# Optimization experiments

Measured on AMD Instinct MI355X. Metric: run time of the kernel, lower is better.

## Reference

```python
import jax, jax.numpy as jnp
import numpy as np

LN_EPS = 1e-5

def _layernorm(x, g, b):
    mu = jnp.mean(x, axis=-1, keepdims=True)
    var = jnp.mean(jnp.square(x - mu), axis=-1, keepdims=True)
    return (x - mu) * jax.lax.rsqrt(var + LN_EPS) * g + b


def setup_inputs() -> dict:
    key = jax.random.key(0)
    ks = jax.random.split(key, 8)
    B, N, F = 2, 100000, 128
    E, G = 400000, 10
    EMB, C = 32, 128
    features = jax.random.normal(ks[0], (B, N, F), dtype=jnp.float32)
    edge_index = jax.random.randint(ks[1], (2, E), 0, N, dtype=jnp.int32)
    lengths = jnp.full((G,), N // G, dtype=jnp.int32)
    emb_table = jax.random.normal(ks[2], (128, EMB), dtype=jnp.float32)
    W_in = jax.random.normal(ks[3], (F - 1 + EMB, C), dtype=jnp.float32) * (1.0 / np.sqrt(F - 1 + EMB))
    b_in = jnp.zeros((C,), jnp.float32)
    g_in = jnp.ones((C,), jnp.float32)
    beta_in = jnp.zeros((C,), jnp.float32)
    msg_W = jax.random.normal(ks[4], (3, C, C), dtype=jnp.float32) * (1.0 / np.sqrt(C))
    msg_b = jnp.zeros((3, C), jnp.float32)
    msg_g = jnp.ones((3, C), jnp.float32)
    msg_beta = jnp.zeros((3, C), jnp.float32)
    W_proj = jax.random.normal(ks[5], (C, 1), dtype=jnp.float32) * (1.0 / np.sqrt(C))
    b_proj = jnp.zeros((1,), jnp.float32)
    return {"features": features, "edge_index": edge_index, "lengths": lengths,
            "emb_table": emb_table, "W_in": W_in, "b_in": b_in, "g_in": g_in, "beta_in": beta_in,
            "msg_W": msg_W, "msg_b": msg_b, "msg_g": msg_g, "msg_beta": msg_beta,
            "W_proj": W_proj, "b_proj": b_proj}


def reference(features, edge_index, lengths, emb_table, W_in, b_in, g_in, beta_in,
              msg_W, msg_b, msg_g, msg_beta, W_proj, b_proj):
    B, N, F = features.shape
    rows, cols = edge_index[0], edge_index[1]

    # row-normalized sparse adjacency values (no grad path in original: torch.no_grad)
    ones = jnp.ones(rows.shape[0], dtype=features.dtype)
    deg = jax.ops.segment_sum(ones, rows, num_segments=N)
    vals = 1.0 / jnp.clip(deg, 1.0)[rows]  # [E]
    vals = jax.lax.stop_gradient(vals)

    # embedding input layer
    op = jnp.clip(features[..., 0].astype(jnp.int32), 0, emb_table.shape[0] - 1)  # [B,N]
    x = jnp.concatenate([emb_table[op], features[..., 1:]], axis=-1)  # [B,N,F-1+emb]
    x = _layernorm(jax.nn.silu(x @ W_in + b_in), g_in, beta_in)  # [B,N,C]

    # sparse message passing: agg[i] = sum_j A[i,j] x[j]
    for l in range(msg_W.shape[0]):
        msg = x[:, cols, :] * vals[None, :, None]  # [B,E,C]
        agg = jnp.zeros_like(x).at[:, rows, :].add(msg)  # scatter-sum to rows
        x = _layernorm(jax.nn.silu(agg @ msg_W[l] + msg_b[l]), msg_g[l], msg_beta[l])

    # ragged graph pooling over node axis
    G = lengths.shape[0]
    index = jnp.asarray(np.repeat(np.arange(G), np.asarray(lengths)))  # [N]
    pooled = jax.ops.segment_sum(x.transpose(1, 0, 2), index, num_segments=G)  # [G,B,C]
    runtimes = pooled @ W_proj + b_proj  # [G,B,1]
    return runtimes[..., 0]  # [G,B]
```

## Files before the change

### kernel.cpp

```cpp
#include <hip/hip_runtime.h>
#include <cstddef>

#define LN_EPS 1e-5f
typedef unsigned short u16;
typedef unsigned int u32;
typedef __attribute__((ext_vector_type(8))) short bf16x8;
typedef __attribute__((ext_vector_type(4))) float f32x4;

constexpr int SCAN_T = 256, SCAN_V = 8, SCAN_ELEMS = SCAN_T * SCAN_V;
constexpr int KP = 136;

__device__ inline u16 f2bf(float f) {
    u32 u = __float_as_uint(f);
    u += 0x7FFFu + ((u >> 16) & 1u);
    return (u16)(u >> 16);
}
__device__ inline float bf2f(u16 h) { return __uint_as_float((u32)h << 16); }

__device__ inline void acc_u4(float* a, uint4 u) {
    a[0] += bf2f((u16)(u.x & 0xFFFF)); a[1] += bf2f((u16)(u.x >> 16));
    a[2] += bf2f((u16)(u.y & 0xFFFF)); a[3] += bf2f((u16)(u.y >> 16));
    a[4] += bf2f((u16)(u.z & 0xFFFF)); a[5] += bf2f((u16)(u.z >> 16));
    a[6] += bf2f((u16)(u.w & 0xFFFF)); a[7] += bf2f((u16)(u.w >> 16));
}

__global__ __launch_bounds__(256) void k_deg(const int* __restrict__ rows,
                                             int* __restrict__ deg, int E) {
    int e = blockIdx.x * 256 + threadIdx.x;
    if (e < E) atomicAdd(&deg[rows[e]], 1);
}

__global__ __launch_bounds__(256) void k_invdeg(const int* __restrict__ deg,
                                                float* __restrict__ invdeg, int N) {
    int i = blockIdx.x * 256 + threadIdx.x;
    if (i < N) invdeg[i] = 1.0f / (float)max(deg[i], 1);
}

__global__ __launch_bounds__(SCAN_T) void k_scan1(const int* __restrict__ deg,
                                                  int* __restrict__ row_ptr,
                                                  int* __restrict__ bsum, int N) {
    __shared__ int ts[SCAN_T];
    int t = threadIdx.x;
    int base = blockIdx.x * SCAN_ELEMS;
    int v[SCAN_V];
    int s = 0;
    #pragma unroll
    for (int j = 0; j < SCAN_V; ++j) {
        int i = base + t * SCAN_V + j;
        v[j] = (i < N) ? deg[i] : 0;
        s += v[j];
    }
    ts[t] = s;
    __syncthreads();
    for (int off = 1; off < SCAN_T; off <<= 1) {
        int val = (t >= off) ? ts[t - off] : 0;
        __syncthreads();
        ts[t] += val;
        __syncthreads();
    }
    int excl = (t > 0) ? ts[t - 1] : 0;
    #pragma unroll
    for (int j = 0; j < SCAN_V; ++j) {
        int i = base + t * SCAN_V + j;
        if (i < N) row_ptr[i] = excl;
        excl += v[j];
    }
    if (t == SCAN_T - 1) bsum[blockIdx.x] = ts[SCAN_T - 1];
}

__global__ void k_scan2(int* __restrict__ bsum, int nb, int* __restrict__ row_ptr, int N) {
    int run = 0;
    for (int i = 0; i < nb; ++i) {
        int v = bsum[i];
        bsum[i] = run;
        run += v;
    }
    row_ptr[N] = run;
}

__global__ __launch_bounds__(SCAN_T) void k_scan3(int* __restrict__ row_ptr,
                                                  const int* __restrict__ bsum, int N) {
    int add = bsum[blockIdx.x];
    int base = blockIdx.x * SCAN_ELEMS;
    #pragma unroll
    for (int j = 0; j < SCAN_V; ++j) {
        int i = base + threadIdx.x * SCAN_V + j;
        if (i < N) row_ptr[i] += add;
    }
}

__global__ __launch_bounds__(256) void k_copy_cursor(const int* __restrict__ row_ptr,
                                                     int* __restrict__ cursor, int N) {
    int i = blockIdx.x * 256 + threadIdx.x;
    if (i < N) cursor[i] = row_ptr[i];
}

__global__ __launch_bounds__(256) void k_bucket(const int* __restrict__ rows,
                                                const int* __restrict__ cols,
                                                int* __restrict__ cursor,
                                                int* __restrict__ col_sorted, int E) {
    int e = blockIdx.x * 256 + threadIdx.x;
    if (e < E) {
        int r = rows[e];
        int pos = atomicAdd(&cursor[r], 1);
        col_sorted[pos] = cols[e];
    }
}

__global__ __launch_bounds__(256) void k_wprep(const float* __restrict__ W_in,
                                               const float* __restrict__ msg_W,
                                               u16* __restrict__ Wt_in,
                                               u16* __restrict__ Wt_msg) {
    int idx = blockIdx.x * 256 + threadIdx.x;
    const int t1 = 128 * KP;
    if (idx < t1) {
        int c = idx / KP, k = idx % KP;
        float v = (k >= 1 && k < 128) ? W_in[(31 + k) * 128 + c] : 0.f;
        Wt_in[idx] = f2bf(v);
    } else {
        idx -= t1;
        if (idx < 3 * 128 * KP) {
            int l = idx / (128 * KP);
            int r = idx % (128 * KP);
            int c = r / KP, k = r % KP;
            Wt_msg[idx] = (k < 128) ? f2bf(msg_W[l * 16384 + k * 128 + c]) : (u16)0;
        }
    }
}

__global__ __launch_bounds__(128) void k_eproj(const float* __restrict__ W_in,
                                               const float* __restrict__ emb,
                                               float* __restrict__ E_proj) {
    __shared__ float es[32];
    int op = blockIdx.x, c = threadIdx.x;
    if (c < 32) es[c] = emb[op * 32 + c];
    __syncthreads();
    float s = 0.f;
    #pragma unroll
    for (int j = 0; j < 32; ++j) s = fmaf(es[j], W_in[j * 128 + c], s);
    E_proj[op * 128 + c] = s;
}

__global__ __launch_bounds__(256) void k_input_mfma(
    const float* __restrict__ features, const float* __restrict__ E_proj,
    const u16* __restrict__ Wt,
    const float* __restrict__ bias, const float* __restrict__ gain,
    const float* __restrict__ beta, u16* __restrict__ x, int M, int ntiles)
{
    __shared__ u16 A[64 * KP];
    __shared__ u16 Wl[128 * KP];
    __shared__ int ops[64];
    const int tid = threadIdx.x;
    const int lane = tid & 63, w = tid >> 6;
    const int r = tid >> 2, q = tid & 3;

    {
        const uint4* src = (const uint4*)Wt;
        uint4* dst = (uint4*)Wl;
        const int n16 = 128 * KP / 8;
        for (int i = tid; i < n16; i += 256) dst[i] = src[i];
    }
    float bsr[8], gsr[8], btr[8];
    #pragma unroll
    for (int t = 0; t < 8; ++t) {
        int col = t * 16 + (lane & 15);
        bsr[t] = bias[col]; gsr[t] = gain[col]; btr[t] = beta[col];
    }

    for (int tile = blockIdx.x; tile < ntiles; tile += gridDim.x) {
        const int node0 = tile * 64;
        __syncthreads();
        {
            int rg = min(node0 + r, M - 1);
            const float* fr = features + (size_t)rg * 128 + q * 32;
            u32 pk[16];
            float4 v0 = ((const float4*)fr)[0];
            if (q == 0) {
                int op = (int)v0.x;
                op = op < 0 ? 0 : (op > 127 ? 127 : op);
                ops[r] = op;
            }
            pk[0] = (u32)f2bf(v0.x) | ((u32)f2bf(v0.y) << 16);
            pk[1] = (u32)f2bf(v0.z) | ((u32)f2bf(v0.w) << 16);
            #pragma unroll
            for (int j = 1; j < 8; ++j) {
                float4 v = ((const float4*)fr)[j];
                pk[2 * j]     = (u32)f2bf(v.x) | ((u32)f2bf(v.y) << 16);
                pk[2 * j + 1] = (u32)f2bf(v.z) | ((u32)f2bf(v.w) << 16);
            }
            uint4* dst = (uint4*)&A[r * KP + q * 32];
            #pragma unroll
            for (int j = 0; j < 4; ++j)
                dst[j] = make_uint4(pk[4 * j], pk[4 * j + 1], pk[4 * j + 2], pk[4 * j + 3]);
        }
        __syncthreads();

        const int arow = w * 16 + (lane & 15);
        const int kq = (lane >> 4) * 8;
        bf16x8 a[4];
        #pragma unroll
        for (int kt = 0; kt < 4; ++kt)
            a[kt] = *(const bf16x8*)&A[arow * KP + kt * 32 + kq];
        f32x4 acc[8];
        #pragma unroll
        for (int t = 0; t < 8; ++t) {
            int bcol = t * 16 + (lane & 15);
            f32x4 c4 = {0.f, 0.f, 0.f, 0.f};
            #pragma unroll
            for (int kt = 0; kt < 4; ++kt) {
                bf16x8 b = *(const bf16x8*)&Wl[bcol * KP + kt * 32 + kq];
                c4 = __builtin_amdgcn_mfma_f32_16x16x32_bf16(a[kt], b, c4, 0, 0, 0);
            }
            acc[t] = c4;
        }
        int opr[4];
        #pragma unroll
        for (int i = 0; i < 4; ++i) opr[i] = ops[w * 16 + (lane >> 4) * 4 + i];
        float s[4] = {0, 0, 0, 0}, sq[4] = {0, 0, 0, 0};
        #pragma unroll
        for (int t = 0; t < 8; ++t) {
            int col = t * 16 + (lane & 15);
            #pragma unroll
            for (int i = 0; i < 4; ++i) {
                float aY = acc[t][i] + bsr[t] + E_proj[opr[i] * 128 + col];
                float y = aY / (1.0f + __expf(-aY));
                acc[t][i] = y;
                s[i] += y;
                sq[i] = fmaf(y, y, sq[i]);
            }
        }
        #pragma unroll
        for (int m = 1; m <= 8; m <<= 1) {
            #pragma unroll
            for (int i = 0; i < 4; ++i) {
                s[i] += __shfl_xor(s[i], m);
                sq[i] += __shfl_xor(sq[i], m);
            }
        }
        #pragma unroll
        for (int i = 0; i < 4; ++i) {
            float mu = s[i] * (1.0f / 128.0f);
            float var = sq[i] * (1.0f / 128.0f) - mu * mu;
            float inv = rsqrtf(var + LN_EPS);
            int rg = node0 + w * 16 + (lane >> 4) * 4 + i;
            if (rg < M) {
                u16* xr = x + (size_t)rg * 128;
                #pragma unroll
                for (int t = 0; t < 8; ++t) {
                    int col = t * 16 + (lane & 15);
                    xr[col] = f2bf((acc[t][i] - mu) * inv * gsr[t] + btr[t]);
                }
            }
        }
    }
}

__global__ __launch_bounds__(256) void k_mp_mfma(
    const int* __restrict__ row_ptr, const int* __restrict__ col_sorted,
    const float* __restrict__ invdeg, const u16* __restrict__ xin,
    const u16* __restrict__ Wt, const float* __restrict__ bias,
    const float* __restrict__ gain, const float* __restrict__ beta,
    u16* __restrict__ xout, int N, int M, int ntiles)
{
    __shared__ u16 A[64 * KP];
    __shared__ u16 Wl[128 * KP];
    const int tid = threadIdx.x;
    const int lane = tid & 63, w = tid >> 6;
    const int r = tid >> 2, q = tid & 3;

    {
        const uint4* src = (const uint4*)Wt;
        uint4* dst = (uint4*)Wl;
        const int n16 = 128 * KP / 8;
        for (int i = tid; i < n16; i += 256) dst[i] = src[i];
    }
    float bsr[8], gsr[8], btr[8];
    #pragma unroll
    for (int t = 0; t < 8; ++t) {
        int col = t * 16 + (lane & 15);
        bsr[t] = bias[col]; gsr[t] = gain[col]; btr[t] = beta[col];
    }

    for (int tile = blockIdx.x; tile < ntiles; tile += gridDim.x) {
        const int node0 = tile * 64;
        __syncthreads();
        {
            int rg = min(node0 + r, M - 1);
            int b = rg / N;
            int nrow = rg - b * N;
            int e0 = row_ptr[nrow], e1 = row_ptr[nrow + 1];
            float sc = invdeg[nrow];
            const u32* xb = (const u32*)xin + (size_t)b * N * 64 + q * 16;
            float fa[32];
            #pragma unroll
            for (int j = 0; j < 32; ++j) fa[j] = 0.f;
            int e = e0;
            for (; e + 2 <= e1; e += 2) {
                int c0 = col_sorted[e], c1 = col_sorted[e + 1];
                const uint4* p0 = (const uint4*)(xb + (size_t)c0 * 64);
                const uint4* p1 = (const uint4*)(xb + (size_t)c1 * 64);
                uint4 u0 = p0[0], u1 = p0[1], u2 = p0[2], u3 = p0[3];
                uint4 w0 = p1[0], w1 = p1[1], w2 = p1[2], w3 = p1[3];
                acc_u4(fa + 0, u0);  acc_u4(fa + 8, u1);
                acc_u4(fa + 16, u2); acc_u4(fa + 24, u3);
                acc_u4(fa + 0, w0);  acc_u4(fa + 8, w1);
                acc_u4(fa + 16, w2); acc_u4(fa + 24, w3);
            }
            if (e < e1) {
                const uint4* p0 = (const uint4*)(xb + (size_t)col_sorted[e] * 64);
                uint4 u0 = p0[0], u1 = p0[1], u2 = p0[2], u3 = p0[3];
                acc_u4(fa + 0, u0);  acc_u4(fa + 8, u1);
                acc_u4(fa + 16, u2); acc_u4(fa + 24, u3);
            }
            u32 pk[16];
            #pragma unroll
            for (int j = 0; j < 16; ++j)
                pk[j] = (u32)f2bf(fa[2 * j] * sc) | ((u32)f2bf(fa[2 * j + 1] * sc) << 16);
            uint4* dst = (uint4*)&A[r * KP + q * 32];
            #pragma unroll
            for (int j = 0; j < 4; ++j)
                dst[j] = make_uint4(pk[4 * j], pk[4 * j + 1], pk[4 * j + 2], pk[4 * j + 3]);
        }
        __syncthreads();

        const int arow = w * 16 + (lane & 15);
        const int kq = (lane >> 4) * 8;
        bf16x8 a[4];
        #pragma unroll
        for (int kt = 0; kt < 4; ++kt)
            a[kt] = *(const bf16x8*)&A[arow * KP + kt * 32 + kq];
        f32x4 acc[8];
        #pragma unroll
        for (int t = 0; t < 8; ++t) {
            int bcol = t * 16 + (lane & 15);
            f32x4 c4 = {0.f, 0.f, 0.f, 0.f};
            #pragma unroll
            for (int kt = 0; kt < 4; ++kt) {
                bf16x8 b = *(const bf16x8*)&Wl[bcol * KP + kt * 32 + kq];
                c4 = __builtin_amdgcn_mfma_f32_16x16x32_bf16(a[kt], b, c4, 0, 0, 0);
            }
            acc[t] = c4;
        }
        float s[4] = {0, 0, 0, 0}, sq[4] = {0, 0, 0, 0};
        #pragma unroll
        for (int t = 0; t < 8; ++t) {
            #pragma unroll
            for (int i = 0; i < 4; ++i) {
                float aY = acc[t][i] + bsr[t];
                float y = aY / (1.0f + __expf(-aY));
                acc[t][i] = y;
                s[i] += y;
                sq[i] = fmaf(y, y, sq[i]);
            }
        }
        #pragma unroll
        for (int m = 1; m <= 8; m <<= 1) {
            #pragma unroll
            for (int i = 0; i < 4; ++i) {
                s[i] += __shfl_xor(s[i], m);
                sq[i] += __shfl_xor(sq[i], m);
            }
        }
        #pragma unroll
        for (int i = 0; i < 4; ++i) {
            float mu = s[i] * (1.0f / 128.0f);
            float var = sq[i] * (1.0f / 128.0f) - mu * mu;
            float inv = rsqrtf(var + LN_EPS);
            int rg = node0 + w * 16 + (lane >> 4) * 4 + i;
            if (rg < M) {
                u16* xr = xout + (size_t)rg * 128;
                #pragma unroll
                for (int t = 0; t < 8; ++t) {
                    int col = t * 16 + (lane & 15);
                    xr[col] = f2bf((acc[t][i] - mu) * inv * gsr[t] + btr[t]);
                }
            }
        }
    }
}

__global__ __launch_bounds__(64) void k_pool(
    const u16* __restrict__ x, const int* __restrict__ lengths,
    float* __restrict__ pooled, int N, int B, int G, int SPLIT)
{
    int blk = blockIdx.x;
    int split = blk % SPLIT;
    int gb = blk / SPLIT;
    int b = gb % B, g = gb / B;
    int lane = threadIdx.x;
    int start = 0;
    for (int i = 0; i < g; ++i) start += lengths[i];
    int len = lengths[g];
    int chunk = (len + SPLIT - 1) / SPLIT;
    int n0 = start + split * chunk;
    int n1 = min(start + len, n0 + chunk);
    const u32* xb = (const u32*)x + (size_t)b * N * 64;
    float sx = 0.f, sy = 0.f;
    int n = n0;
    for (; n + 8 <= n1; n += 8) {
        u32 v0 = xb[(size_t)(n + 0) * 64 + lane];
        u32 v1 = xb[(size_t)(n + 1) * 64 + lane];
        u32 v2 = xb[(size_t)(n + 2) * 64 + lane];
        u32 v3 = xb[(size_t)(n + 3) * 64 + lane];
        u32 v4 = xb[(size_t)(n + 4) * 64 + lane];
        u32 v5 = xb[(size_t)(n + 5) * 64 + lane];
        u32 v6 = xb[(size_t)(n + 6) * 64 + lane];
        u32 v7 = xb[(size_t)(n + 7) * 64 + lane];
        sx += bf2f((u16)(v0 & 0xFFFF)) + bf2f((u16)(v1 & 0xFFFF)) +
              bf2f((u16)(v2 & 0xFFFF)) + bf2f((u16)(v3 & 0xFFFF)) +
              bf2f((u16)(v4 & 0xFFFF)) + bf2f((u16)(v5 & 0xFFFF)) +
              bf2f((u16)(v6 & 0xFFFF)) + bf2f((u16)(v7 & 0xFFFF));
        sy += bf2f((u16)(v0 >> 16)) + bf2f((u16)(v1 >> 16)) +
              bf2f((u16)(v2 >> 16)) + bf2f((u16)(v3 >> 16)) +
              bf2f((u16)(v4 >> 16)) + bf2f((u16)(v5 >> 16)) +
              bf2f((u16)(v6 >> 16)) + bf2f((u16)(v7 >> 16));
    }
    for (; n < n1; ++n) {
        u32 v = xb[(size_t)n * 64 + lane];
        sx += bf2f((u16)(v & 0xFFFF));
        sy += bf2f((u16)(v >> 16));
    }
    if (n1 > n0) {
        atomicAdd(&pooled[(g * B + b) * 128 + lane * 2 + 0], sx);
        atomicAdd(&pooled[(g * B + b) * 128 + lane * 2 + 1], sy);
    }
}

__global__ __launch_bounds__(128) void k_proj(
    const float* __restrict__ pooled, const float* __restrict__ Wp,
    const float* __restrict__ bp, float* __restrict__ out, int GB)
{
    int gb = blockIdx.x;
    int tid = threadIdx.x;
    float v = pooled[gb * 128 + tid] * Wp[tid];
    v += __shfl_down(v, 32);
    v += __shfl_down(v, 16);
    v += __shfl_down(v, 8);
    v += __shfl_down(v, 4);
    v += __shfl_down(v, 2);
    v += __shfl_down(v, 1);
    __shared__ float red[2];
    if ((tid & 63) == 0) red[tid >> 6] = v;
    __syncthreads();
    if (tid == 0) out[gb] = red[0] + red[1] + bp[0];
}

extern "C" void kernel_launch(void* const* d_in, const int* in_sizes, int n_in,
                              void* d_out, int out_size, void* d_ws, size_t ws_size,
                              hipStream_t stream) {
    const float* features = (const float*)d_in[0];
    const int* edge_index = (const int*)d_in[1];
    const int* lengths    = (const int*)d_in[2];
    const float* emb      = (const float*)d_in[3];
    const float* W_in     = (const float*)d_in[4];
    const float* b_in     = (const float*)d_in[5];
    const float* g_in     = (const float*)d_in[6];
    const float* beta_in  = (const float*)d_in[7];
    const float* msg_W    = (const float*)d_in[8];
    const float* msg_b    = (const float*)d_in[9];
    const float* msg_g    = (const float*)d_in[10];
    const float* msg_beta = (const float*)d_in[11];
    const float* W_proj   = (const float*)d_in[12];
    const float* b_proj   = (const float*)d_in[13];
    float* out = (float*)d_out;

    const int E = in_sizes[1] / 2;
    const int G = in_sizes[2];
    const int B = out_size / G;
    const int C = in_sizes[5];
    const int F = 128;
    const int N = in_sizes[0] / (B * F);
    const int M = B * N;
    const int L = in_sizes[9] / C;

    const int* rows = edge_index;
    const int* cols = edge_index + E;

    u16* buf0   = (u16*)d_ws;
    u16* buf1   = buf0 + (size_t)M * 128;
    u16* Wt_in  = buf1 + (size_t)M * 128;
    u16* Wt_msg = Wt_in + 128 * KP;
    float* E_proj = (float*)(Wt_msg + 3 * 128 * KP);
    float* invdeg = E_proj + 128 * 128;
    int*   deg    = (int*)(invdeg + N);
    float* pooled = (float*)(deg + N);
    int*   row_ptr = (int*)(pooled + (size_t)G * B * 128);
    int*   col_sorted = row_ptr + N + 1;
    int*   bsum   = col_sorted + E;

    const int nb_scan = (N + SCAN_ELEMS - 1) / SCAN_ELEMS;
    const int ntiles = (M + 63) / 64;
    const int grid_g = ntiles < 768 ? ntiles : 768;

    {
        int total = 4 * 128 * KP;
        k_wprep<<<(total + 255) / 256, 256, 0, stream>>>(W_in, msg_W, Wt_in, Wt_msg);
        k_eproj<<<128, 128, 0, stream>>>(W_in, emb, E_proj);
    }

    hipMemsetAsync(deg, 0, (size_t)N * sizeof(int), stream);
    k_deg<<<(E + 255) / 256, 256, 0, stream>>>(rows, deg, E);
    k_invdeg<<<(N + 255) / 256, 256, 0, stream>>>(deg, invdeg, N);
    k_scan1<<<nb_scan, SCAN_T, 0, stream>>>(deg, row_ptr, bsum, N);
    k_scan2<<<1, 1, 0, stream>>>(bsum, nb_scan, row_ptr, N);
    k_scan3<<<nb_scan, SCAN_T, 0, stream>>>(row_ptr, bsum, N);
    k_copy_cursor<<<(N + 255) / 256, 256, 0, stream>>>(row_ptr, deg, N);
    k_bucket<<<(E + 255) / 256, 256, 0, stream>>>(rows, cols, deg, col_sorted, E);

    k_input_mfma<<<grid_g, 256, 0, stream>>>(features, E_proj, Wt_in,
                                             b_in, g_in, beta_in, buf0, M, ntiles);

    u16* bufs[2] = {buf0, buf1};
    int cur = 0;
    for (int l = 0; l < L; ++l) {
        k_mp_mfma<<<grid_g, 256, 0, stream>>>(row_ptr, col_sorted, invdeg,
                                              bufs[cur], Wt_msg + (size_t)l * 128 * KP,
                                              msg_b + (size_t)l * C, msg_g + (size_t)l * C,
                                              msg_beta + (size_t)l * C,
                                              bufs[1 - cur], N, M, ntiles);
        cur = 1 - cur;
    }

    const int SPLIT = 128;
    hipMemsetAsync(pooled, 0, (size_t)G * B * 128 * sizeof(float), stream);
    k_pool<<<G * B * SPLIT, 64, 0, stream>>>(bufs[cur], lengths, pooled, N, B, G, SPLIT);
    k_proj<<<G * B, 128, 0, stream>>>(pooled, W_proj, b_proj, out, G * B);
}
```

Measured before the change: 392.2 us.

## Drop LDS staging; build MFMA fragments in registers and read weights from global

The input and message-passing kernels no longer stage the A tile and weight matrix in shared memory. Each lane now gathers or loads exactly the bf16 fragment it feeds to the MFMA, and B fragments are read directly from the unpadded global weight array, which should hit in cache. This removes the block-wide barriers and the LDS footprint, allowing more resident blocks (launch bounds of 4 and a larger grid). The cost is redundant global/L2 weight reads per tile and a less coalesced per-lane gather layout for neighbor rows.

```diff
diff --git a/kernel.cpp b/kernel.cpp
--- a/kernel.cpp
+++ b/kernel.cpp
@@ -8,7 +8,6 @@
 typedef __attribute__((ext_vector_type(4))) float f32x4;
 
 constexpr int SCAN_T = 256, SCAN_V = 8, SCAN_ELEMS = SCAN_T * SCAN_V;
-constexpr int KP = 136;
 
 __device__ inline u16 f2bf(float f) {
     u32 u = __float_as_uint(f);
@@ -112,18 +111,18 @@
                                                u16* __restrict__ Wt_in,
                                                u16* __restrict__ Wt_msg) {
     int idx = blockIdx.x * 256 + threadIdx.x;
-    const int t1 = 128 * KP;
+    const int t1 = 128 * 128;
     if (idx < t1) {
-        int c = idx / KP, k = idx % KP;
-        float v = (k >= 1 && k < 128) ? W_in[(31 + k) * 128 + c] : 0.f;
+        int c = idx >> 7, k = idx & 127;
+        float v = (k >= 1) ? W_in[(31 + k) * 128 + c] : 0.f;
         Wt_in[idx] = f2bf(v);
     } else {
         idx -= t1;
-        if (idx < 3 * 128 * KP) {
-            int l = idx / (128 * KP);
-            int r = idx % (128 * KP);
-            int c = r / KP, k = r % KP;
-            Wt_msg[idx] = (k < 128) ? f2bf(msg_W[l * 16384 + k * 128 + c]) : (u16)0;
+        if (idx < 3 * 128 * 128) {
+            int l = idx / (128 * 128);
+            int r = idx & (128 * 128 - 1);
+            int c = r >> 7, k = r & 127;
+            Wt_msg[idx] = f2bf(msg_W[l * 16384 + k * 128 + c]);
         }
     }
 }
@@ -141,85 +140,68 @@
     E_proj[op * 128 + c] = s;
 }
 
-__global__ __launch_bounds__(256) void k_input_mfma(
+__global__ __launch_bounds__(256, 4) void k_input_mfma(
     const float* __restrict__ features, const float* __restrict__ E_proj,
     const u16* __restrict__ Wt,
     const float* __restrict__ bias, const float* __restrict__ gain,
     const float* __restrict__ beta, u16* __restrict__ x, int M, int ntiles)
 {
-    __shared__ u16 A[64 * KP];
-    __shared__ u16 Wl[128 * KP];
-    __shared__ int ops[64];
     const int tid = threadIdx.x;
     const int lane = tid & 63, w = tid >> 6;
-    const int r = tid >> 2, q = tid & 3;
-
-    {
-        const uint4* src = (const uint4*)Wt;
-        uint4* dst = (uint4*)Wl;
-        const int n16 = 128 * KP / 8;
-        for (int i = tid; i < n16; i += 256) dst[i] = src[i];
-    }
+    const int l15 = lane & 15;
+    const int kq = (lane >> 4) * 8;
+
     float bsr[8], gsr[8], btr[8];
     #pragma unroll
     for (int t = 0; t < 8; ++t) {
-        int col = t * 16 + (lane & 15);
+        int col = t * 16 + l15;
         bsr[t] = bias[col]; gsr[t] = gain[col]; btr[t] = beta[col];
     }
 
     for (int tile = blockIdx.x; tile < ntiles; tile += gridDim.x) {
         const int node0 = tile * 64;
-        __syncthreads();
-        {
-            int rg = min(node0 + r, M - 1);
-            const float* fr = features + (size_t)rg * 128 + q * 32;
-            u32 pk[16];
-            float4 v0 = ((const float4*)fr)[0];
-            if (q == 0) {
-                int op = (int)v0.x;
-                op = op < 0 ? 0 : (op > 127 ? 127 : op);
-                ops[r] = op;
-            }
-            pk[0] = (u32)f2bf(v0.x) | ((u32)f2bf(v0.y) << 16);
-            pk[1] = (u32)f2bf(v0.z) | ((u32)f2bf(v0.w) << 16);
-            #pragma unroll
-            for (int j = 1; j < 8; ++j) {
-                float4 v = ((const float4*)fr)[j];
-                pk[2 * j]     = (u32)f2bf(v.x) | ((u32)f2bf(v.y) << 16);
-                pk[2 * j + 1] = (u32)f2bf(v.z) | ((u32)f2bf(v.w) << 16);
-            }
-            uint4* dst = (uint4*)&A[r * KP + q * 32];
-            #pragma unroll
-            for (int j = 0; j < 4; ++j)
-                dst[j] = make_uint4(pk[4 * j], pk[4 * j + 1], pk[4 * j + 2], pk[4 * j + 3]);
-        }
-        __syncthreads();
-
-        const int arow = w * 16 + (lane & 15);
-        const int kq = (lane >> 4) * 8;
+        const int arow = w * 16 + l15;
+        int rg = min(node0 + arow, M - 1);
+
         bf16x8 a[4];
         #pragma unroll
-        for (int kt = 0; kt < 4; ++kt)
-            a[kt] = *(const bf16x8*)&A[arow * KP + kt * 32 + kq];
+        for (int kt = 0; kt < 4; ++kt) {
+            const float* fp = features + (size_t)rg * 128 + kt * 32 + kq;
+            float4 v0 = ((const float4*)fp)[0];
+            float4 v1 = ((const float4*)fp)[1];
+            union { u32 p[4]; bf16x8 v; } cvt;
+            cvt.p[0] = (u32)f2bf(v0.x) | ((u32)f2bf(v0.y) << 16);
+            cvt.p[1] = (u32)f2bf(v0.z) | ((u32)f2bf(v0.w) << 16);
+            cvt.p[2] = (u32)f2bf(v1.x) | ((u32)f2bf(v1.y) << 16);
+            cvt.p[3] = (u32)f2bf(v1.z) | ((u32)f2bf(v1.w) << 16);
+            a[kt] = cvt.v;
+        }
+
         f32x4 acc[8];
         #pragma unroll
         for (int t = 0; t < 8; ++t) {
-            int bcol = t * 16 + (lane & 15);
+            const u16* wp = Wt + (size_t)(t * 16 + l15) * 128 + kq;
             f32x4 c4 = {0.f, 0.f, 0.f, 0.f};
             #pragma unroll
             for (int kt = 0; kt < 4; ++kt) {
-                bf16x8 b = *(const bf16x8*)&Wl[bcol * KP + kt * 32 + kq];
+                bf16x8 b = *(const bf16x8*)(wp + kt * 32);
                 c4 = __builtin_amdgcn_mfma_f32_16x16x32_bf16(a[kt], b, c4, 0, 0, 0);
             }
             acc[t] = c4;
         }
+
         int opr[4];
         #pragma unroll
-        for (int i = 0; i < 4; ++i) opr[i] = ops[w * 16 + (lane >> 4) * 4 + i];
+        for (int i = 0; i < 4; ++i) {
+            int rr = min(node0 + w * 16 + (lane >> 4) * 4 + i, M - 1);
+            int op = (int)features[(size_t)rr * 128];
+            opr[i] = op < 0 ? 0 : (op > 127 ? 127 : op);
+        }
+
         float s[4] = {0, 0, 0, 0}, sq[4] = {0, 0, 0, 0};
         #pragma unroll
         for (int t = 0; t < 8; ++t) {
-            int col = t * 16 + (lane & 15);
+            int col = t * 16 + l15;
             #pragma unroll
             for (int i = 0; i < 4; ++i) {
                 float aY = acc[t][i] + bsr[t] + E_proj[opr[i] * 128 + col];
@@ -242,105 +224,93 @@
             float mu = s[i] * (1.0f / 128.0f);
             float var = sq[i] * (1.0f / 128.0f) - mu * mu;
             float inv = rsqrtf(var + LN_EPS);
-            int rg = node0 + w * 16 + (lane >> 4) * 4 + i;
-            if (rg < M) {
-                u16* xr = x + (size_t)rg * 128;
+            int rg2 = node0 + w * 16 + (lane >> 4) * 4 + i;
+            if (rg2 < M) {
+                u16* xr = x + (size_t)rg2 * 128;
                 #pragma unroll
-                for (int t = 0; t < 8; ++t) {
-                    int col = t * 16 + (lane & 15);
-                    xr[col] = f2bf((acc[t][i] - mu) * inv * gsr[t] + btr[t]);
-                }
-            }
-        }
-    }
-}
-
-__global__ __launch_bounds__(256) void k_mp_mfma(
+                for (int t = 0; t < 8; ++t)
+                    xr[t * 16 + l15] = f2bf((acc[t][i] - mu) * inv * gsr[t] + btr[t]);
+            }
+        }
+    }
+}
+
+__global__ __launch_bounds__(256, 4) void k_mp_mfma(
     const int* __restrict__ row_ptr, const int* __restrict__ col_sorted,
     const float* __restrict__ invdeg, const u16* __restrict__ xin,
     const u16* __restrict__ Wt, const float* __restrict__ bias,
     const float* __restrict__ gain, const float* __restrict__ beta,
     u16* __restrict__ xout, int N, int M, int ntiles)
 {
-    __shared__ u16 A[64 * KP];
-    __shared__ u16 Wl[128 * KP];
     const int tid = threadIdx.x;
     const int lane = tid & 63, w = tid >> 6;
-    const int r = tid >> 2, q = tid & 3;
-
-    {
-        const uint4* src = (const uint4*)Wt;
-        uint4* dst = (uint4*)Wl;
-        const int n16 = 128 * KP / 8;
-        for (int i = tid; i < n16; i += 256) dst[i] = src[i];
-    }
+    const int l15 = lane & 15;
+    const int q4 = lane >> 4;
+    const int kq = q4 * 8;
+
     float bsr[8], gsr[8], btr[8];
     #pragma unroll
     for (int t = 0; t < 8; ++t) {
-        int col = t * 16 + (lane & 15);
+        int col = t * 16 + l15;
         bsr[t] = bias[col]; gsr[t] = gain[col]; btr[t] = beta[col];
     }
 
     for (int tile = blockIdx.x; tile < ntiles; tile += gridDim.x) {
         const int node0 = tile * 64;
-        __syncthreads();
-        {
-            int rg = min(node0 + r, M - 1);
-            int b = rg / N;
-            int nrow = rg - b * N;
-            int e0 = row_ptr[nrow], e1 = row_ptr[nrow + 1];
-            float sc = invdeg[nrow];
-            const u32* xb = (const u32*)xin + (size_t)b * N * 64 + q * 16;
-            float fa[32];
-            #pragma unroll
-            for (int j = 0; j < 32; ++j) fa[j] = 0.f;
-            int e = e0;
-            for (; e + 2 <= e1; e += 2) {
-                int c0 = col_sorted[e], c1 = col_sorted[e + 1];
-                const uint4* p0 = (const uint4*)(xb + (size_t)c0 * 64);
-                const uint4* p1 = (const uint4*)(xb + (size_t)c1 * 64);
-                uint4 u0 = p0[0], u1 = p0[1], u2 = p0[2], u3 = p0[3];
-                uint4 w0 = p1[0], w1 = p1[1], w2 = p1[2], w3 = p1[3];
-                acc_u4(fa + 0, u0);  acc_u4(fa + 8, u1);
-                acc_u4(fa + 16, u2); acc_u4(fa + 24, u3);
-                acc_u4(fa + 0, w0);  acc_u4(fa + 8, w1);
-                acc_u4(fa + 16, w2); acc_u4(fa + 24, w3);
-            }
-            if (e < e1) {
-                const uint4* p0 = (const uint4*)(xb + (size_t)col_sorted[e] * 64);
-                uint4 u0 = p0[0], u1 = p0[1], u2 = p0[2], u3 = p0[3];
-                acc_u4(fa + 0, u0);  acc_u4(fa + 8, u1);
-                acc_u4(fa + 16, u2); acc_u4(fa + 24, u3);
-            }
-            u32 pk[16];
-            #pragma unroll
-            for (int j = 0; j < 16; ++j)
-                pk[j] = (u32)f2bf(fa[2 * j] * sc) | ((u32)f2bf(fa[2 * j + 1] * sc) << 16);
-            uint4* dst = (uint4*)&A[r * KP + q * 32];
+        const int arow = w * 16 + l15;
+        int rg = min(node0 + arow, M - 1);
+        int b = rg / N;
+        int nrow = rg - b * N;
+        int e0 = row_ptr[nrow], e1 = row_ptr[nrow + 1];
+        float sc = invdeg[nrow];
+        const u32* xb = (const u32*)xin + (size_t)b * N * 64;
+
+        float fa[32];
+        #pragma unroll
+        for (int j = 0; j < 32; ++j) fa[j] = 0.f;
+        int e = e0;
+        for (; e + 2 <= e1; e += 2) {
+            int c0 = col_sorted[e], c1 = col_sorted[e + 1];
+            const uint4* p0 = (const uint4*)(xb + (size_t)c0 * 64);
+            const uint4* p1 = (const uint4*)(xb + (size_t)c1 * 64);
+            uint4 u0 = p0[q4], u1 = p0[4 + q4], u2 = p0[8 + q4], u3 = p0[12 + q4];
+            uint4 w0 = p1[q4], w1 = p1[4 + q4], w2 = p1[8 + q4], w3 = p1[12 + q4];
+            acc_u4(fa + 0, u0);  acc_u4(fa + 8, u1);
+            acc_u4(fa + 16, u2); acc_u4(fa + 24, u3);
+            acc_u4(fa + 0, w0);  acc_u4(fa + 8, w1);
+            acc_u4(fa + 16, w2); acc_u4(fa + 24, w3);
+        }
+        if (e < e1) {
+            const uint4* p0 = (const uint4*)(xb + (size_t)col_sorted[e] * 64);
+            uint4 u0 = p0[q4], u1 = p0[4 + q4], u2 = p0[8 + q4], u3 = p0[12 + q4];
+            acc_u4(fa + 0, u0);  acc_u4(fa + 8, u1);
+            acc_u4(fa + 16, u2); acc_u4(fa + 24, u3);
+        }
+
+        bf16x8 a[4];
+        #pragma unroll
+        for (int kt = 0; kt < 4; ++kt) {
+            union { u32 p[4]; bf16x8 v; } cvt;
             #pragma unroll
             for (int j = 0; j < 4; ++j)
-                dst[j] = make_uint4(pk[4 * j], pk[4 * j + 1], pk[4 * j + 2], pk[4 * j + 3]);
-        }
-        __syncthreads();
-
-        const int arow = w * 16 + (lane & 15);
-        const int kq = (lane >> 4) * 8;
-        bf16x8 a[4];
-        #pragma unroll
-        for (int kt = 0; kt < 4; ++kt)
-            a[kt] = *(const bf16x8*)&A[arow * KP + kt * 32 + kq];
+                cvt.p[j] = (u32)f2bf(fa[kt * 8 + 2 * j] * sc) |
+                           ((u32)f2bf(fa[kt * 8 + 2 * j + 1] * sc) << 16);
+            a[kt] = cvt.v;
+        }
+
         f32x4 acc[8];
         #pragma unroll
         for (int t = 0; t < 8; ++t) {
-            int bcol = t * 16 + (lane & 15);
+            const u16* wp = Wt + (size_t)(t * 16 + l15) * 128 + kq;
             f32x4 c4 = {0.f, 0.f, 0.f, 0.f};
             #pragma unroll
             for (int kt = 0; kt < 4; ++kt) {
-                bf16x8 b = *(const bf16x8*)&Wl[bcol * KP + kt * 32 + kq];
-                c4 = __builtin_amdgcn_mfma_f32_16x16x32_bf16(a[kt], b, c4, 0, 0, 0);
+                bf16x8 bfr = *(const bf16x8*)(wp + kt * 32);
+                c4 = __builtin_amdgcn_mfma_f32_16x16x32_bf16(a[kt], bfr, c4, 0, 0, 0);
             }
             acc[t] = c4;
         }
+
         float s[4] = {0, 0, 0, 0}, sq[4] = {0, 0, 0, 0};
         #pragma unroll
         for (int t = 0; t < 8; ++t) {
@@ -366,14 +336,12 @@
             float mu = s[i] * (1.0f / 128.0f);
             float var = sq[i] * (1.0f / 128.0f) - mu * mu;
             float inv = rsqrtf(var + LN_EPS);
-            int rg = node0 + w * 16 + (lane >> 4) * 4 + i;
-            if (rg < M) {
-                u16* xr = xout + (size_t)rg * 128;
+            int rg2 = node0 + w * 16 + (lane >> 4) * 4 + i;
+            if (rg2 < M) {
+                u16* xr = xout + (size_t)rg2 * 128;
                 #pragma unroll
-                for (int t = 0; t < 8; ++t) {
-                    int col = t * 16 + (lane & 15);
-                    xr[col] = f2bf((acc[t][i] - mu) * inv * gsr[t] + btr[t]);
-                }
+                for (int t = 0; t < 8; ++t)
+                    xr[t * 16 + l15] = f2bf((acc[t][i] - mu) * inv * gsr[t] + btr[t]);
             }
         }
     }
@@ -479,8 +447,8 @@
     u16* buf0   = (u16*)d_ws;
     u16* buf1   = buf0 + (size_t)M * 128;
     u16* Wt_in  = buf1 + (size_t)M * 128;
-    u16* Wt_msg = Wt_in + 128 * KP;
-    float* E_proj = (float*)(Wt_msg + 3 * 128 * KP);
+    u16* Wt_msg = Wt_in + 128 * 128;
+    float* E_proj = (float*)(Wt_msg + 3 * 128 * 128);
     float* invdeg = E_proj + 128 * 128;
     int*   deg    = (int*)(invdeg + N);
     float* pooled = (float*)(deg + N);
@@ -490,10 +458,10 @@
 
     const int nb_scan = (N + SCAN_ELEMS - 1) / SCAN_ELEMS;
     const int ntiles = (M + 63) / 64;
-    const int grid_g = ntiles < 768 ? ntiles : 768;
+    const int grid_g = ntiles < 1280 ? ntiles : 1280;
 
     {
-        int total = 4 * 128 * KP;
+        int total = 4 * 128 * 128;
         k_wprep<<<(total + 255) / 256, 256, 0, stream>>>(W_in, msg_W, Wt_in, Wt_msg);
         k_eproj<<<128, 128, 0, stream>>>(W_in, emb, E_proj);
     }
@@ -514,7 +482,7 @@
     int cur = 0;
     for (int l = 0; l < L; ++l) {
         k_mp_mfma<<<grid_g, 256, 0, stream>>>(row_ptr, col_sorted, invdeg,
-                                              bufs[cur], Wt_msg + (size_t)l * 128 * KP,
+                                              bufs[cur], Wt_msg + (size_t)l * 128 * 128,
                                               msg_b + (size_t)l * C, msg_g + (size_t)l * C,
                                               msg_beta + (size_t)l * C,
                                               bufs[1 - cur], N, M, ntiles);
```

Result: slower. 706.5 us (+80.2%).
